# Kernel tuning notes

Hardware: AMD Instinct MI355X
Metric: run time of the kernel (lower is better)

The kernel has to match this reference:

```python
import jax, jax.numpy as jnp
import numpy as np

T, B, I, H, A = 2048, 2, 40, 44, 262144  # seq_len, batch, input, hidden, max action len
E = 2 * H  # 88, branch embedding dim; E + I == 128 (Linear in_features)


def setup_inputs() -> dict:
    key = jax.random.key(0)
    ks = jax.random.split(key, 11)
    s = 1.0 / np.sqrt(H).astype(np.float32)
    u = lambda k, shape: jax.random.uniform(k, shape, jnp.float32, -s, s)
    sl = 1.0 / np.sqrt(E + I).astype(np.float32)
    return {
        "x": jax.random.normal(ks[0], (T, B, I), jnp.float32),
        "h0": jax.random.normal(ks[1], (1, B, H), jnp.float32),
        "c0": jax.random.normal(ks[2], (1, B, H), jnp.float32),
        "action": jax.random.normal(ks[3], (B, A, I), jnp.float32),
        "act_length": jax.random.randint(ks[4], (B,), 1, A + 1, jnp.int32),
        "W_ih": u(ks[5], (4 * H, I)),
        "W_hh": u(ks[6], (4 * H, H)),
        "b_ih": u(ks[7], (4 * H,)),
        "b_hh": u(ks[8], (4 * H,)),
        "W_v": jax.random.uniform(ks[9], (1, E + I), jnp.float32, -sl, sl),
        "b_v": jax.random.uniform(ks[10], (1,), jnp.float32, -sl, sl),
    }


def _lstm_final(x, h0, c0, W_ih, W_hh, b_ih, b_hh):
    # single-layer LSTM, returns final (h, c), each (B, H); torch gate order i,f,g,o
    def step(carry, xt):
        h, c = carry
        g = xt @ W_ih.T + b_ih + h @ W_hh.T + b_hh  # (B, 4H)
        i, f, gg, o = jnp.split(g, 4, axis=-1)
        c = jax.nn.sigmoid(f) * c + jax.nn.sigmoid(i) * jnp.tanh(gg)
        h = jax.nn.sigmoid(o) * jnp.tanh(c)
        return (h, c), None
    (h, c), _ = jax.lax.scan(step, (h0[0], c0[0]), x)
    return h, c


def reference(x, h0, c0, action, act_length, W_ih, W_hh, b_ih, b_hh, W_v, b_v):
    h, c = _lstm_final(x, h0, c0, W_ih, W_hh, b_ih, b_hh)
    emb = jnp.concatenate([h, c], axis=-1)  # (B, 88) == brench_embeding[0]
    w = W_v[0]
    w_e, w_a = w[:E], w[E:]  # split Linear(128->1) weight over [embed | act]
    # val[b, i] = emb[b].w_e + action[b, i].w_a + b_v  (fused ragged linear)
    vals = (emb @ w_e)[:, None] + jnp.einsum("bad,d->ba", action, w_a) + b_v[0]
    mask = jnp.arange(A)[None, :] < act_length[:, None]  # ragged lengths
    return jnp.where(mask, vals, 0.0)
```

## Files before the change

### kernel.cpp

```cpp
#include <hip/hip_runtime.h>

typedef float v2f __attribute__((ext_vector_type(2)));
typedef float v4f __attribute__((ext_vector_type(4)));

#define T_STEPS 2048
#define BATCH   2
#define IDIM    40
#define HDIM    44
#define GDIM    176
#define ADIM    262144
#define EDIM    88
#define NEG_L   (-1.4426950408889634f)
#define NEG_2L  (-2.8853900817779268f)

__global__ __launch_bounds__(192) void xproj_kernel(
    const float* __restrict__ x,
    const float* __restrict__ W_ih,
    const float* __restrict__ b_ih,
    const float* __restrict__ b_hh,
    float* __restrict__ xproj)
{
    const int tb = blockIdx.x;
    const int gi = threadIdx.x;
    __shared__ __align__(16) float xs[IDIM];
    if (threadIdx.x < IDIM) xs[threadIdx.x] = x[(size_t)tb * IDIM + threadIdx.x];
    __syncthreads();
    if (gi < GDIM) {
        const float* wr = W_ih + gi * IDIM;
        float a0 = 0.f, a1 = 0.f;
        #pragma unroll
        for (int i = 0; i < IDIM; i += 4) {
            float4 wv = *(const float4*)&wr[i];
            float4 xv = *(const float4*)&xs[i];
            a0 += wv.x * xv.x + wv.z * xv.z;
            a1 += wv.y * xv.y + wv.w * xv.w;
        }
        const float scale = (gi >= 2 * HDIM && gi < 3 * HDIM) ? NEG_2L : NEG_L;
        xproj[(size_t)tb * GDIM + gi] = scale * (a0 + a1 + b_ih[gi] + b_hh[gi]);
    }
}

__global__ __launch_bounds__(128)
__attribute__((amdgpu_waves_per_eu(1, 1)))
void lstm_kernel(
    const float* __restrict__ xproj,
    const float* __restrict__ h0,
    const float* __restrict__ c0,
    const float* __restrict__ W_hh,
    const float* __restrict__ W_v,
    const float* __restrict__ b_v,
    float* __restrict__ base_out)
{
    const int b    = blockIdx.x;
    const int tid  = threadIdx.x;
    const int wave = tid >> 6;
    const int lane = tid & 63;
    const int sub  = lane & 31;
    const int half = lane >> 5;
    const bool act = (sub < 22);
    const int subc = act ? sub : 21;
    const int unit = wave * 22 + subc;

    __shared__ __align__(16) float h_sh[64];
    __shared__ float part[2];

    const int row0 = half ? (2 * HDIM + unit) : unit;
    const int row1 = row0 + HDIM;
    const float sc0 = half ? NEG_2L : NEG_L;
    const float sc1 = NEG_L;

    v2f w0[22], w1[22];
    {
        const float* r0p = W_hh + (size_t)row0 * HDIM;
        const float* r1p = W_hh + (size_t)row1 * HDIM;
        #pragma unroll
        for (int k = 0; k < 22; ++k) {
            w0[k] = ((const v2f*)r0p)[k] * sc0;
            w1[k] = ((const v2f*)r1p)[k] * sc1;
        }
    }

    float c = c0[b * HDIM + unit];
    if (tid < HDIM) h_sh[tid] = h0[b * HDIM + tid];
    if (tid >= HDIM && tid < 64) h_sh[tid] = 0.f;
    __syncthreads();

    v2f hp[22];
    #pragma unroll
    for (int k = 0; k < 11; ++k) {
        v4f t = ((const v4f*)h_sh)[k];
        hp[2 * k]     = __builtin_shufflevector(t, t, 0, 1);
        hp[2 * k + 1] = __builtin_shufflevector(t, t, 2, 3);
    }

    const float* xp = xproj + (size_t)b * GDIM;
    #define LDX(d0, d1, s) { const float* _a = xp + (size_t)(s) * (BATCH * GDIM); \
        d0 = _a[row0]; d1 = _a[row1]; }
    float r0v, r1v, p0v, p1v;
    LDX(r0v, r1v, 0) LDX(p0v, p1v, 1)

    float hval = 0.f;

    #pragma unroll 1
    for (int step = 0; step < T_STEPS; ++step) {
        v2f a0 = {r0v, 0.f}, a1 = {r1v, 0.f};
        #pragma unroll
        for (int k = 0; k < 22; ++k) {
            a0 = __builtin_elementwise_fma(w0[k], hp[k], a0);
            a1 = __builtin_elementwise_fma(w1[k], hp[k], a1);
        }
        float y0 = a0.x + a0.y;
        float y1 = a1.x + a1.y;

        float v0 = __builtin_amdgcn_rcpf(1.0f + __builtin_amdgcn_exp2f(y0));
        float v1 = __builtin_amdgcn_rcpf(1.0f + __builtin_amdgcn_exp2f(y1));

        float o0 = __shfl_xor(v0, 32);
        float o1 = __shfl_xor(v1, 32);

        float s_i = half ? o0 : v0;
        float s_f = half ? o1 : v1;
        float w_g = half ? v0 : o0;
        float s_o = half ? v1 : o1;

        float t_g = __builtin_fmaf(2.0f, w_g, -1.0f);
        c = s_f * c + s_i * t_g;
        float w_c = __builtin_amdgcn_rcpf(1.0f + __builtin_amdgcn_exp2f(c * NEG_2L));
        hval = __builtin_fmaf(s_o + s_o, w_c, -s_o);

        if (act && half == 0) h_sh[unit] = hval;
        __syncthreads();

        #pragma unroll
        for (int k = 0; k < 11; ++k) {
            v4f t = ((const v4f*)h_sh)[k];
            hp[2 * k]     = __builtin_shufflevector(t, t, 0, 1);
            hp[2 * k + 1] = __builtin_shufflevector(t, t, 2, 3);
        }

        r0v = p0v; r1v = p1v;
        const int ns = (step + 2 < T_STEPS) ? step + 2 : (T_STEPS - 1);
        LDX(p0v, p1v, ns)
    }
    #undef LDX

    float p = 0.f;
    if (act && half == 0) p = hval * W_v[unit] + c * W_v[HDIM + unit];
    #pragma unroll
    for (int off = 32; off; off >>= 1) p += __shfl_down(p, off);
    if (lane == 0) part[wave] = p;
    __syncthreads();
    if (tid == 0) base_out[b] = part[0] + part[1] + b_v[0];
}

__global__ __launch_bounds__(256) void action_kernel(
    const float* __restrict__ action,
    const int*   __restrict__ act_length,
    const float* __restrict__ W_v,
    const float* __restrict__ base,
    float* __restrict__ out)
{
    const int idx = blockIdx.x * 256 + threadIdx.x;
    const int b = idx >> 18;
    const int a = idx & (ADIM - 1);
    if (a >= act_length[b]) { out[idx] = 0.f; return; }
    const float* row = action + (size_t)idx * IDIM;
    float a0 = 0.f, a1 = 0.f;
    #pragma unroll
    for (int i = 0; i < IDIM; i += 4) {
        float4 av = *(const float4*)&row[i];
        a0 += av.x * W_v[EDIM + i + 0] + av.z * W_v[EDIM + i + 2];
        a1 += av.y * W_v[EDIM + i + 1] + av.w * W_v[EDIM + i + 3];
    }
    out[idx] = base[b] + a0 + a1;
}

extern "C" void kernel_launch(void* const* d_in, const int* in_sizes, int n_in,
                              void* d_out, int out_size, void* d_ws, size_t ws_size,
                              hipStream_t stream) {
    const float* x        = (const float*)d_in[0];
    const float* h0       = (const float*)d_in[1];
    const float* c0       = (const float*)d_in[2];
    const float* action   = (const float*)d_in[3];
    const int*   act_len  = (const int*)  d_in[4];
    const float* W_ih     = (const float*)d_in[5];
    const float* W_hh     = (const float*)d_in[6];
    const float* b_ih     = (const float*)d_in[7];
    const float* b_hh     = (const float*)d_in[8];
    const float* W_v      = (const float*)d_in[9];
    const float* b_v      = (const float*)d_in[10];
    float* out = (float*)d_out;

    float* xproj = (float*)d_ws;
    float* base  = xproj + (size_t)T_STEPS * BATCH * GDIM;

    xproj_kernel<<<dim3(T_STEPS * BATCH), dim3(192), 0, stream>>>(
        x, W_ih, b_ih, b_hh, xproj);
    lstm_kernel<<<dim3(BATCH), dim3(128), 0, stream>>>(
        xproj, h0, c0, W_hh, W_v, b_v, base);
    action_kernel<<<dim3((BATCH * ADIM) / 256), dim3(256), 0, stream>>>(
        action, act_len, W_v, base, out);
}
```

Before: 641.3 us.

## Split LSTM recurrence into own-wave bpermute and foreign-wave LDS halves with double buffering

Each wave now gets its own 22 hidden units through ds_bpermute within the wave, and reads only the other wave's 22 units from a double-buffered shared array. The matvec is split so the own-half FMAs come first and can overlap the barrier and the LDS reads of the foreign half. This is meant to shorten the per-step critical path on the serial 2048-step recurrence. The cost is 22 bpermute instructions per step and more live registers. The h layout changes to padded 32-slot per-wave blocks.

```diff
diff --git a/kernel.cpp b/kernel.cpp
--- a/kernel.cpp
+++ b/kernel.cpp
@@ -60,8 +60,9 @@
     const bool act = (sub < 22);
     const int subc = act ? sub : 21;
     const int unit = wave * 22 + subc;
-
-    __shared__ __align__(16) float h_sh[64];
+    const bool act2 = act && (half == 0);
+
+    __shared__ __align__(16) float hsh[2][64];
     __shared__ float part[2];
 
     const int row0 = half ? (2 * HDIM + unit) : unit;
@@ -69,28 +70,40 @@
     const float sc0 = half ? NEG_2L : NEG_L;
     const float sc1 = NEG_L;
 
-    v2f w0[22], w1[22];
+    const int ownb  = wave * 22;
+    const int forb  = (wave ^ 1) * 22;
+    const int wslot = wave * 32;
+    const int fslot = (wave ^ 1) * 32;
+
+    v2f w0o[11], w0f[11], w1o[11], w1f[11];
     {
         const float* r0p = W_hh + (size_t)row0 * HDIM;
         const float* r1p = W_hh + (size_t)row1 * HDIM;
         #pragma unroll
-        for (int k = 0; k < 22; ++k) {
-            w0[k] = ((const v2f*)r0p)[k] * sc0;
-            w1[k] = ((const v2f*)r1p)[k] * sc1;
+        for (int k = 0; k < 11; ++k) {
+            w0o[k] = ((const v2f*)(r0p + ownb))[k] * sc0;
+            w0f[k] = ((const v2f*)(r0p + forb))[k] * sc0;
+            w1o[k] = ((const v2f*)(r1p + ownb))[k] * sc1;
+            w1f[k] = ((const v2f*)(r1p + forb))[k] * sc1;
         }
     }
 
     float c = c0[b * HDIM + unit];
-    if (tid < HDIM) h_sh[tid] = h0[b * HDIM + tid];
-    if (tid >= HDIM && tid < 64) h_sh[tid] = 0.f;
+    if (tid < HDIM) hsh[0][(tid / 22) * 32 + (tid % 22)] = h0[b * HDIM + tid];
     __syncthreads();
 
-    v2f hp[22];
-    #pragma unroll
-    for (int k = 0; k < 11; ++k) {
-        v4f t = ((const v4f*)h_sh)[k];
-        hp[2 * k]     = __builtin_shufflevector(t, t, 0, 1);
-        hp[2 * k + 1] = __builtin_shufflevector(t, t, 2, 3);
+    v2f hpO[11], hpF[11];
+    {
+        const v4f* ob = (const v4f*)&hsh[0][wslot];
+        const v4f* fb = (const v4f*)&hsh[0][fslot];
+        #pragma unroll
+        for (int k = 0; k < 11; ++k) {
+            v4f oq = ob[k >> 1], fq = fb[k >> 1];
+            hpO[k] = (k & 1) ? __builtin_shufflevector(oq, oq, 2, 3)
+                             : __builtin_shufflevector(oq, oq, 0, 1);
+            hpF[k] = (k & 1) ? __builtin_shufflevector(fq, fq, 2, 3)
+                             : __builtin_shufflevector(fq, fq, 0, 1);
+        }
     }
 
     const float* xp = xproj + (size_t)b * GDIM;
@@ -103,21 +116,26 @@
 
     #pragma unroll 1
     for (int step = 0; step < T_STEPS; ++step) {
-        v2f a0 = {r0v, 0.f}, a1 = {r1v, 0.f};
-        #pragma unroll
-        for (int k = 0; k < 22; ++k) {
-            a0 = __builtin_elementwise_fma(w0[k], hp[k], a0);
-            a1 = __builtin_elementwise_fma(w1[k], hp[k], a1);
-        }
-        float y0 = a0.x + a0.y;
-        float y1 = a1.x + a1.y;
+        v2f a0o = {r0v, 0.f}, a1o = {r1v, 0.f};
+        #pragma unroll
+        for (int k = 0; k < 11; ++k) {
+            a0o = __builtin_elementwise_fma(w0o[k], hpO[k], a0o);
+            a1o = __builtin_elementwise_fma(w1o[k], hpO[k], a1o);
+        }
+        v2f a0f = {0.f, 0.f}, a1f = {0.f, 0.f};
+        #pragma unroll
+        for (int k = 0; k < 11; ++k) {
+            a0f = __builtin_elementwise_fma(w0f[k], hpF[k], a0f);
+            a1f = __builtin_elementwise_fma(w1f[k], hpF[k], a1f);
+        }
+        float y0 = (a0o.x + a0o.y) + (a0f.x + a0f.y);
+        float y1 = (a1o.x + a1o.y) + (a1f.x + a1f.y);
 
         float v0 = __builtin_amdgcn_rcpf(1.0f + __builtin_amdgcn_exp2f(y0));
         float v1 = __builtin_amdgcn_rcpf(1.0f + __builtin_amdgcn_exp2f(y1));
 
         float o0 = __shfl_xor(v0, 32);
         float o1 = __shfl_xor(v1, 32);
-
         float s_i = half ? o0 : v0;
         float s_f = half ? o1 : v1;
         float w_g = half ? v0 : o0;
@@ -128,14 +146,27 @@
         float w_c = __builtin_amdgcn_rcpf(1.0f + __builtin_amdgcn_exp2f(c * NEG_2L));
         hval = __builtin_fmaf(s_o + s_o, w_c, -s_o);
 
-        if (act && half == 0) h_sh[unit] = hval;
+        const int wb = (step + 1) & 1;
+        if (act2) hsh[wb][wslot + sub] = hval;
+
+        const int hb = __float_as_int(hval);
+        float tt[22];
+        #pragma unroll
+        for (int u = 0; u < 22; ++u)
+            tt[u] = __int_as_float(__builtin_amdgcn_ds_bpermute(4 * u, hb));
+        #pragma unroll
+        for (int k = 0; k < 11; ++k) hpO[k] = (v2f){tt[2 * k], tt[2 * k + 1]};
+
         __syncthreads();
 
-        #pragma unroll
-        for (int k = 0; k < 11; ++k) {
-            v4f t = ((const v4f*)h_sh)[k];
-            hp[2 * k]     = __builtin_shufflevector(t, t, 0, 1);
-            hp[2 * k + 1] = __builtin_shufflevector(t, t, 2, 3);
+        {
+            const v4f* fb = (const v4f*)&hsh[wb][fslot];
+            #pragma unroll
+            for (int k = 0; k < 11; ++k) {
+                v4f fq = fb[k >> 1];
+                hpF[k] = (k & 1) ? __builtin_shufflevector(fq, fq, 2, 3)
+                                 : __builtin_shufflevector(fq, fq, 0, 1);
+            }
         }
 
         r0v = p0v; r1v = p1v;
@@ -145,7 +176,7 @@
     #undef LDX
 
     float p = 0.f;
-    if (act && half == 0) p = hval * W_v[unit] + c * W_v[HDIM + unit];
+    if (act2) p = hval * W_v[unit] + c * W_v[HDIM + unit];
     #pragma unroll
     for (int off = 32; off; off >>= 1) p += __shfl_down(p, off);
     if (lane == 0) part[wave] = p;
```

Result: slower. 880.9 us (+37.4%).
